# Performance work log

Hardware: AMD Instinct MI355X
Metric: run time of the kernel (lower is better)

The kernel has to match this reference:

```python
import jax, jax.numpy as jnp
import numpy as np

B, L, D, H, S = 2, 2048, 1024, 16, 4
Dh = D // H
EPS = 1e-5


def setup_inputs() -> dict:
    key = jax.random.key(0)
    ks = jax.random.split(key, 12)
    sc = 0.02
    w = lambda k, shape: (jax.random.normal(k, shape, jnp.float32) * sc)
    M = 2 * S  # number of MHA blocks / dense linears
    inp = {
        "response": jax.random.normal(ks[0], (B, L, D), jnp.float32),
        "mask": jnp.broadcast_to(jnp.tril(jnp.ones((L, L), bool)), (B, L, L)),
        "Wq": w(ks[1], (M, D, D)), "bq": w(ks[2], (M, D)),
        "Wk": w(ks[3], (M, D, D)), "bk": w(ks[4], (M, D)),
        "Wv": w(ks[5], (M, D, D)), "bv": w(ks[6], (M, D)),
        "Wo": w(ks[7], (M, D, D)), "bo": w(ks[8], (M, D)),
        "Wd": w(ks[9], (M, D, D)), "bd": w(ks[10], (M, D)),
    }
    return inp


def _ln(x):
    # fresh LayerNorm(d) with default weight=1, bias=0, eps=1e-5
    m = jnp.mean(x, axis=-1, keepdims=True)
    v = jnp.mean((x - m) ** 2, axis=-1, keepdims=True)
    return (x - m) * jax.lax.rsqrt(v + EPS)


def _linear(x, W, b):
    # torch Linear: x @ W.T + b
    return jnp.einsum('bld,od->blo', x, W) + b


def _mha(x, i, mask, Wq, bq, Wk, bk, Wv, bv, Wo, bo):
    # self-attention: q = k = v = x
    split = lambda y: y.reshape(B, L, H, Dh).transpose(0, 2, 1, 3)  # (B,H,L,Dh)
    q = split(_linear(x, Wq[i], bq[i]))
    k = split(_linear(x, Wk[i], bk[i]))
    v = split(_linear(x, Wv[i], bv[i]))
    scores = jnp.einsum('bhqd,bhkd->bhqk', q, k) / jnp.sqrt(jnp.float32(Dh))
    if mask is not None:
        scores = jnp.where(mask[:, None, :, :], scores, -jnp.inf)
    p = jnp.nan_to_num(jax.nn.softmax(scores, axis=-1))
    o = jnp.einsum('bhqk,bhkd->bhqd', p, v).transpose(0, 2, 1, 3).reshape(B, L, D)
    return _linear(o, Wo[i], bo[i])


def reference(response, mask, Wq, bq, Wk, bk, Wv, bv, Wo, bo, Wd, bd):
    x = response
    for i in range(S):
        # masked self-attention + residual + LN
        x = _ln(x + _mha(x, 2 * i, mask, Wq, bq, Wk, bk, Wv, bv, Wo, bo))
        # encoder-attention sublayer (encMem is None -> unmasked self-attention)
        x = _ln(x + _mha(x, 2 * i + 1, None, Wq, bq, Wk, bk, Wv, bv, Wo, bo))
        # dense: linear[2i](LeakyReLU(linear[2i+1](x)))
        h = jax.nn.leaky_relu(_linear(x, Wd[2 * i + 1], bd[2 * i + 1]), negative_slope=0.01)
        h = _linear(h, Wd[2 * i], bd[2 * i])
        x = _ln(x + h)
    return x
```

## Files before the change

kernel.cpp:

```cpp
#include <hip/hip_runtime.h>
#include <stdint.h>
#include <stddef.h>

typedef __attribute__((ext_vector_type(8))) _Float16 f16x8;
typedef __attribute__((ext_vector_type(4))) _Float16 f16x4;
typedef __attribute__((ext_vector_type(4))) float    f32x4;

#define NB 2
#define NL 2048
#define ND 1024
#define NH 16
#define NROWS (NB*NL)

__device__ __forceinline__ void async16(void* lds, const void* g) {
  __builtin_amdgcn_global_load_lds(
      (const __attribute__((address_space(1))) void*)g,
      (__attribute__((address_space(3))) void*)lds, 16, 0, 0);
}

struct CvtArgs { const float* in[6]; _Float16* out[6]; };

__global__ __launch_bounds__(256) void cvt_all(CvtArgs a, int n16, int rn16)
{
  const float* in  = a.in[blockIdx.z];
  _Float16*   out  = a.out[blockIdx.z];
  const int n = (blockIdx.z == 5) ? rn16 : n16;
  for (int i = blockIdx.x * blockDim.x + threadIdx.x; i < n;
       i += gridDim.x * blockDim.x) {
    const f32x4* src = (const f32x4*)in + 4 * (size_t)i;
    f32x4 v0 = __builtin_nontemporal_load(src);
    f32x4 v1 = __builtin_nontemporal_load(src + 1);
    f32x4 v2 = __builtin_nontemporal_load(src + 2);
    f32x4 v3 = __builtin_nontemporal_load(src + 3);
    f16x8 o0 = {(_Float16)v0[0], (_Float16)v0[1], (_Float16)v0[2], (_Float16)v0[3],
                (_Float16)v1[0], (_Float16)v1[1], (_Float16)v1[2], (_Float16)v1[3]};
    f16x8 o1 = {(_Float16)v2[0], (_Float16)v2[1], (_Float16)v2[2], (_Float16)v2[3],
                (_Float16)v3[0], (_Float16)v3[1], (_Float16)v3[2], (_Float16)v3[3]};
    __builtin_nontemporal_store(o0, (f16x8*)out + 2 * (size_t)i);
    __builtin_nontemporal_store(o1, (f16x8*)out + 2 * (size_t)i + 1);
  }
}

struct GArgs {
  const _Float16* A;
  const _Float16* B[3];
  const float*    bias[3];
  void*           out[3];
  int             mode[3];
  int             ksplit;
};

__global__ __launch_bounds__(256, 4) void gemm_bt(GArgs ga)
{
  __shared__ _Float16 As[128 * 64];
  __shared__ _Float16 Bs[128 * 64];
  const int tid = threadIdx.x;
  const int w = tid >> 6, l = tid & 63;
  const int ql = l & 15, g = l >> 4;
  const int z = blockIdx.z;
  const int widx = ga.ksplit ? 0 : (blockIdx.x >> 3);
  const _Float16* Bw  = ga.B[widx];
  const float*   bias = ga.bias[widx];
  void*          outp = ga.ksplit ? ga.out[z] : ga.out[widx];
  const int      mode = ga.mode[widx];
  const int kbeg = ga.ksplit ? z * (ND / 2) : 0;
  const int kend = ga.ksplit ? kbeg + ND / 2 : ND;
  const bool dobias = (!ga.ksplit) || (z == 0);
  const int brow = blockIdx.y * 128;
  const int bcol = (blockIdx.x & 7) * 128;
  const int wm = w >> 1, wn = w & 1;
  f32x4 acc[4][4] = {};

  const int srow = w * 32 + (l >> 3);
  const int scol = ((l & 7) ^ (l >> 3)) << 3;
  const _Float16* Ag = ga.A + (size_t)(brow + srow) * ND + scol;
  const _Float16* Bg = Bw   + (size_t)(bcol + srow) * ND + scol;

  for (int k0 = kbeg; k0 < kend; k0 += 64) {
    {
      _Float16* AsW = &As[w * 2048];
      _Float16* BsW = &Bs[w * 2048];
#pragma unroll
      for (int i = 0; i < 4; ++i) {
        async16(AsW + i * 512, Ag + (size_t)i * 8 * ND + k0);
        async16(BsW + i * 512, Bg + (size_t)i * 8 * ND + k0);
      }
    }
    asm volatile("s_waitcnt vmcnt(0)" ::: "memory");
    __builtin_amdgcn_s_barrier();
    __builtin_amdgcn_s_setprio(1);
#pragma unroll
    for (int ks = 0; ks < 64; ks += 32) {
      const int cx = (ks + g * 8) ^ ((ql & 7) << 3);
      f16x8 af[4], bf[4];
#pragma unroll
      for (int mi = 0; mi < 4; ++mi)
        af[mi] = *(const f16x8*)&As[(wm * 64 + mi * 16 + ql) * 64 + cx];
#pragma unroll
      for (int nj = 0; nj < 4; ++nj)
        bf[nj] = *(const f16x8*)&Bs[(wn * 64 + nj * 16 + ql) * 64 + cx];
#pragma unroll
      for (int mi = 0; mi < 4; ++mi)
#pragma unroll
        for (int nj = 0; nj < 4; ++nj)
          acc[mi][nj] = __builtin_amdgcn_mfma_f32_16x16x32_f16(
              af[mi], bf[nj], acc[mi][nj], 0, 0, 0);
    }
    __builtin_amdgcn_s_setprio(0);
    asm volatile("s_waitcnt lgkmcnt(0)" ::: "memory");
    __builtin_amdgcn_s_barrier();
  }

  const int colb = bcol + wn * 64;
  const int rowb = brow + wm * 64 + g * 4;
  if (mode == 3) {
    _Float16* vt = (_Float16*)outp;
    const int bb = rowb >> 11;
#pragma unroll
    for (int nj = 0; nj < 4; ++nj) {
      const int col = colb + nj * 16 + ql;
      const float bv = bias[col];
      const int hh = col >> 6, d = col & 63;
      _Float16* vrow = vt + ((size_t)((bb * NH + hh) * 64 + d)) * NL;
#pragma unroll
      for (int mi = 0; mi < 4; ++mi) {
        const int krow = (rowb + mi * 16) & (NL - 1);
        f16x4 o;
#pragma unroll
        for (int r = 0; r < 4; ++r) o[r] = (_Float16)(acc[mi][nj][r] + bv);
        *(f16x4*)(vrow + krow) = o;
      }
    }
  } else {
    _Float16* oh = (_Float16*)outp;
#pragma unroll
    for (int nj = 0; nj < 4; ++nj) {
      const int col = colb + nj * 16 + ql;
      const float bv = dobias ? bias[col] : 0.f;
#pragma unroll
      for (int mi = 0; mi < 4; ++mi) {
#pragma unroll
        for (int r = 0; r < 4; ++r) {
          float v = acc[mi][nj][r] + bv;
          if (mode == 2) v = v > 0.f ? v : 0.01f * v;
          oh[(size_t)(rowb + mi * 16 + r) * ND + col] = (_Float16)v;
        }
      }
    }
  }
}

template<bool CAUSAL>
__global__ __launch_bounds__(512, 4) void attn_fwd(
    const _Float16* __restrict__ Q, const _Float16* __restrict__ K,
    const _Float16* __restrict__ Vt, _Float16* __restrict__ O)
{
  __shared__ _Float16 kv[3][2][64 * 64];
  __shared__ unsigned int pls[8][8 * 34];
  const int tid = threadIdx.x;
  const int w = tid >> 6, l = tid & 63;
  const int ql = l & 15, g = l >> 4;
  const int bi = blockIdx.x;
  const int within = bi >> 3;
  const int p = (bi & 7) + 8 * (within >> 4);
  const int h = p & 15, b = p >> 4;
  const int qt_raw = within & 15;
  const int qt = (CAUSAL && b) ? (NL / 128 - 1 - qt_raw) : qt_raw;
  const int qrow = qt * 128 + w * 16 + ql;
  const int qmin = qt * 128 + w * 16;

  const _Float16* Qp = Q + (size_t)(b * NL + qrow) * ND + h * 64 + g * 8;
  const f16x8 bq0 = *(const f16x8*)Qp;
  const f16x8 bq1 = *(const f16x8*)(Qp + 32);

  const int srow = w * 8 + (l >> 3);
  const int scol = ((l & 7) ^ (l >> 3)) << 3;
  const _Float16* Kg = K  + ((size_t)(b * NL) + srow) * ND + h * 64 + scol;
  const _Float16* Vg = Vt + ((size_t)((b * NH + h) * 64 + srow)) * NL + scol;

  const int msk  = (ql & 7) << 3;
  const int offA = ql * 64 + ((     g * 8) ^ msk);
  const int offB = ql * 64 + ((32 + g * 8) ^ msk);

  unsigned int* pw = &pls[w][0];
  f32x4 ot[4] = {};
  f32x4 sum_acc = {};
  const f16x8 ones = {(_Float16)1.f, (_Float16)1.f, (_Float16)1.f, (_Float16)1.f,
                      (_Float16)1.f, (_Float16)1.f, (_Float16)1.f, (_Float16)1.f};
  const int ntiles = CAUSAL ? (qt * 2 + 2) : (NL / 64);
  const float SCL = 0.125f * 1.44269504089f;
  const float M2  = 4.0f * 1.44269504089f;

  async16(&kv[0][0][w * 512], Kg);
  async16(&kv[0][1][w * 512], Vg);

  int cbuf = 0, sbuf = 1;
  for (int kt = 0; kt < ntiles; ++kt) {
    const size_t nk0 = (size_t)((kt + 1 < ntiles) ? kt + 1 : kt) * 64;
    async16(&kv[sbuf][0][w * 512], Kg + nk0 * ND);
    async16(&kv[sbuf][1][w * 512], Vg + nk0);
    asm volatile("s_waitcnt vmcnt(2)" ::: "memory");
    __builtin_amdgcn_s_barrier();

    const _Float16* kb = &kv[cbuf][0][0];
    const _Float16* vb = &kv[cbuf][1][0];
    const int k0 = kt * 64;
    f32x4 st[4] = {};
    __builtin_amdgcn_s_setprio(1);
#pragma unroll
    for (int sub = 0; sub < 4; ++sub) {
      const f16x8 a0 = *(const f16x8*)&kb[sub * 1024 + offA];
      const f16x8 a1 = *(const f16x8*)&kb[sub * 1024 + offB];
      st[sub] = __builtin_amdgcn_mfma_f32_16x16x32_f16(a0, bq0, st[sub], 0, 0, 0);
      st[sub] = __builtin_amdgcn_mfma_f32_16x16x32_f16(a1, bq1, st[sub], 0, 0, 0);
    }
    __builtin_amdgcn_s_setprio(0);
    float pv[16];
    if (!CAUSAL || (k0 + 63 <= qmin)) {
#pragma unroll
      for (int sub = 0; sub < 4; ++sub)
#pragma unroll
        for (int r = 0; r < 4; ++r)
          pv[sub * 4 + r] = exp2f(__builtin_fmaf(st[sub][r], SCL, -M2));
    } else {
#pragma unroll
      for (int sub = 0; sub < 4; ++sub)
#pragma unroll
        for (int r = 0; r < 4; ++r) {
          float p2 = exp2f(__builtin_fmaf(st[sub][r], SCL, -M2));
          if ((k0 + sub * 16 + g * 4 + r) > qrow) p2 = 0.f;
          pv[sub * 4 + r] = p2;
        }
    }

#pragma unroll
    for (int sub = 0; sub < 2; ++sub) {
      uint2 uu;
      uu.x = __builtin_bit_cast(unsigned int,
                __builtin_amdgcn_cvt_pkrtz(pv[sub * 4 + 0], pv[sub * 4 + 1]));
      uu.y = __builtin_bit_cast(unsigned int,
                __builtin_amdgcn_cvt_pkrtz(pv[sub * 4 + 2], pv[sub * 4 + 3]));
      *(uint2*)&pw[(sub * 4 + g) * 34 + 2 * ql] = uu;
    }
    {
      uint2 lo = *(const uint2*)&pw[(2 * g    ) * 34 + 2 * ql];
      uint2 hi = *(const uint2*)&pw[(2 * g + 1) * 34 + 2 * ql];
      uint4 ui; ui.x = lo.x; ui.y = lo.y; ui.z = hi.x; ui.w = hi.y;
      const f16x8 pf = __builtin_bit_cast(f16x8, ui);
      __builtin_amdgcn_s_setprio(1);
#pragma unroll
      for (int dt = 0; dt < 4; ++dt) {
        const f16x8 vf = *(const f16x8*)&vb[dt * 1024 + offA];
        ot[dt] = __builtin_amdgcn_mfma_f32_16x16x32_f16(vf, pf, ot[dt], 0, 0, 0);
      }
      sum_acc = __builtin_amdgcn_mfma_f32_16x16x32_f16(ones, pf, sum_acc, 0, 0, 0);
      __builtin_amdgcn_s_setprio(0);
    }
#pragma unroll
    for (int sub = 2; sub < 4; ++sub) {
      uint2 uu;
      uu.x = __builtin_bit_cast(unsigned int,
                __builtin_amdgcn_cvt_pkrtz(pv[sub * 4 + 0], pv[sub * 4 + 1]));
      uu.y = __builtin_bit_cast(unsigned int,
                __builtin_amdgcn_cvt_pkrtz(pv[sub * 4 + 2], pv[sub * 4 + 3]));
      *(uint2*)&pw[((sub - 2) * 4 + g) * 34 + 2 * ql] = uu;
    }
    {
      uint2 lo = *(const uint2*)&pw[(2 * g    ) * 34 + 2 * ql];
      uint2 hi = *(const uint2*)&pw[(2 * g + 1) * 34 + 2 * ql];
      uint4 ui; ui.x = lo.x; ui.y = lo.y; ui.z = hi.x; ui.w = hi.y;
      const f16x8 pf = __builtin_bit_cast(f16x8, ui);
      __builtin_amdgcn_s_setprio(1);
#pragma unroll
      for (int dt = 0; dt < 4; ++dt) {
        const f16x8 vf = *(const f16x8*)&vb[dt * 1024 + offB];
        ot[dt] = __builtin_amdgcn_mfma_f32_16x16x32_f16(vf, pf, ot[dt], 0, 0, 0);
      }
      sum_acc = __builtin_amdgcn_mfma_f32_16x16x32_f16(ones, pf, sum_acc, 0, 0, 0);
      __builtin_amdgcn_s_setprio(0);
    }
    cbuf = sbuf;
    sbuf = sbuf + 1 == 3 ? 0 : sbuf + 1;
  }

  const float inv = 1.f / sum_acc[0];
#pragma unroll
  for (int dt = 0; dt < 4; ++dt) {
    f16x4 o;
#pragma unroll
    for (int r = 0; r < 4; ++r) o[r] = (_Float16)(ot[dt][r] * inv);
    *(f16x4*)(O + (size_t)(b * NL + qrow) * ND + h * 64 + dt * 16 + g * 4) = o;
  }
}

template<bool FINAL>
__global__ __launch_bounds__(256) void resid_ln(
    const _Float16* __restrict__ xh_in, const _Float16* __restrict__ d0,
    const _Float16* __restrict__ d1,
    _Float16* __restrict__ xh_out, float* __restrict__ xf)
{
  const int row = blockIdx.x, tid = threadIdx.x;
  const f16x4 xv = ((const f16x4*)(xh_in + (size_t)row * ND))[tid];
  const f16x4 v0 = ((const f16x4*)(d0 + (size_t)row * ND))[tid];
  const f16x4 v1 = ((const f16x4*)(d1 + (size_t)row * ND))[tid];
  const float a = (float)xv[0] + (float)v0[0] + (float)v1[0];
  const float b = (float)xv[1] + (float)v0[1] + (float)v1[1];
  const float c = (float)xv[2] + (float)v0[2] + (float)v1[2];
  const float d = (float)xv[3] + (float)v0[3] + (float)v1[3];
  float s = a + b + c + d;
  float ss = a * a + b * b + c * c + d * d;
#pragma unroll
  for (int m = 1; m < 64; m <<= 1) {
    s  += __shfl_xor(s, m);
    ss += __shfl_xor(ss, m);
  }
  __shared__ float red[8];
  if ((tid & 63) == 0) { red[tid >> 6] = s; red[4 + (tid >> 6)] = ss; }
  __syncthreads();
  const float S  = red[0] + red[1] + red[2] + red[3];
  const float SS = red[4] + red[5] + red[6] + red[7];
  const float mean = S * (1.0f / ND);
  const float var  = SS * (1.0f / ND) - mean * mean;
  const float rstd = rsqrtf(fmaxf(var, 0.f) + 1e-5f);
  const float ya = (a - mean) * rstd, yb = (b - mean) * rstd;
  const float yc = (c - mean) * rstd, yd = (d - mean) * rstd;
  if (FINAL) {
    float4 y; y.x = ya; y.y = yb; y.z = yc; y.w = yd;
    ((float4*)(xf + (size_t)row * ND))[tid] = y;
  } else {
    f16x4 yh = {(_Float16)ya, (_Float16)yb, (_Float16)yc, (_Float16)yd};
    ((f16x4*)(xh_out + (size_t)row * ND))[tid] = yh;
  }
}

extern "C" void kernel_launch(void* const* d_in, const int* in_sizes, int n_in,
                              void* d_out, int out_size, void* d_ws, size_t ws_size,
                              hipStream_t stream)
{
  (void)in_sizes; (void)n_in; (void)out_size; (void)ws_size;
  const float* response = (const float*)d_in[0];
  const float* Wq = (const float*)d_in[2];
  const float* bq = (const float*)d_in[3];
  const float* Wk = (const float*)d_in[4];
  const float* bk = (const float*)d_in[5];
  const float* Wv = (const float*)d_in[6];
  const float* bv = (const float*)d_in[7];
  const float* Wo = (const float*)d_in[8];
  const float* bo = (const float*)d_in[9];
  const float* Wd = (const float*)d_in[10];
  const float* bd = (const float*)d_in[11];
  float* xf = (float*)d_out;

  const size_t MB = 1024 * 1024;
  char* p = (char*)d_ws;
  _Float16* Wq_h = (_Float16*)(p + 0 * MB);
  _Float16* Wk_h = (_Float16*)(p + 16 * MB);
  _Float16* Wv_h = (_Float16*)(p + 32 * MB);
  _Float16* Wo_h = (_Float16*)(p + 48 * MB);
  _Float16* Wd_h = (_Float16*)(p + 64 * MB);
  _Float16* xh   = (_Float16*)(p + 80 * MB);
  _Float16* Qh   = (_Float16*)(p + 88 * MB);
  _Float16* Kh   = (_Float16*)(p + 96 * MB);
  _Float16* Vth  = (_Float16*)(p + 104 * MB);
  _Float16* Oh   = (_Float16*)(p + 112 * MB);
  _Float16* h1   = Qh;
  _Float16* t0   = (_Float16*)(p + 96 * MB);
  _Float16* t1   = (_Float16*)(p + 104 * MB);

  const int wn16 = 8 * 1024 * 1024 / 16;
  const int rn16 = NROWS * ND / 16;
  CvtArgs ca = { { Wq, Wk, Wv, Wo, Wd, response },
                 { Wq_h, Wk_h, Wv_h, Wo_h, Wd_h, xh } };
  cvt_all<<<dim3(1024, 1, 6), 256, 0, stream>>>(ca, wn16, rn16);

  const dim3 g3(24, NROWS / 128, 1);
  const dim3 gs(8, NROWS / 128, 2);
  const dim3 gf(8, NROWS / 128, 1);
  const dim3 agrid(NL / 128 * NH * NB);

  for (int i = 0; i < 4; ++i) {
    for (int sub = 0; sub < 2; ++sub) {
      const int m = 2 * i + sub;
      const size_t wo = (size_t)m * MB;
      const size_t bf = (size_t)m * 1024;
      GArgs qkv = { xh,
                    { Wq_h + wo, Wk_h + wo, Wv_h + wo },
                    { bq + bf, bk + bf, bv + bf },
                    { Qh, Kh, Vth }, { 0, 0, 3 }, 0 };
      gemm_bt<<<g3, 256, 0, stream>>>(qkv);
      if (sub == 0) attn_fwd<true ><<<agrid, 512, 0, stream>>>(Qh, Kh, Vth, Oh);
      else          attn_fwd<false><<<agrid, 512, 0, stream>>>(Qh, Kh, Vth, Oh);
      GArgs oprj = { Oh,
                     { Wo_h + wo, nullptr, nullptr },
                     { bo + bf, nullptr, nullptr },
                     { t0, t1, nullptr }, { 0, 0, 0 }, 1 };
      gemm_bt<<<gs, 256, 0, stream>>>(oprj);
      resid_ln<false><<<NROWS, 256, 0, stream>>>(xh, t0, t1, xh, nullptr);
    }
    const size_t w1 = (size_t)(2 * i + 1) * MB, b1 = (size_t)(2 * i + 1) * 1024;
    const size_t w0 = (size_t)(2 * i) * MB,     b0 = (size_t)(2 * i) * 1024;
    GArgs f1 = { xh,
                 { Wd_h + w1, nullptr, nullptr },
                 { bd + b1, nullptr, nullptr },
                 { h1, nullptr, nullptr }, { 2, 0, 0 }, 0 };
    gemm_bt<<<gf, 256, 0, stream>>>(f1);
    GArgs f2 = { h1,
                 { Wd_h + w0, nullptr, nullptr },
                 { bd + b0, nullptr, nullptr },
                 { t0, t1, nullptr }, { 0, 0, 0 }, 1 };
    gemm_bt<<<gs, 256, 0, stream>>>(f2);
    if (i == 3) resid_ln<true ><<<NROWS, 256, 0, stream>>>(xh, t0, t1, nullptr, xf);
    else        resid_ln<false><<<NROWS, 256, 0, stream>>>(xh, t0, t1, xh, nullptr);
  }
}
```

Baseline: 1.184 ms.

## Process KV tiles in pairs with double-buffered pair prefetch in attention

The attention loop now handles two 64-key tiles per iteration. The two tiles share one vmcnt(0) wait and one barrier, and the next pair is prefetched into the other half of a 4-slot LDS buffer. The aim is to halve the number of barriers and waits per key and so reduce synchronisation overhead. It also drops the fast path that skipped masking on fully-visible causal tiles, so the causal mask compare now runs on every tile. The extra LDS buffer raises shared memory use, which may reduce occupancy under launch_bounds(512,4).

```diff
diff --git a/kernel.cpp b/kernel.cpp
--- a/kernel.cpp
+++ b/kernel.cpp
@@ -155,7 +155,7 @@
     const _Float16* __restrict__ Q, const _Float16* __restrict__ K,
     const _Float16* __restrict__ Vt, _Float16* __restrict__ O)
 {
-  __shared__ _Float16 kv[3][2][64 * 64];
+  __shared__ _Float16 kv[4][2][64 * 64];
   __shared__ unsigned int pls[8][8 * 34];
   const int tid = threadIdx.x;
   const int w = tid >> 6, l = tid & 63;
@@ -167,7 +167,6 @@
   const int qt_raw = within & 15;
   const int qt = (CAUSAL && b) ? (NL / 128 - 1 - qt_raw) : qt_raw;
   const int qrow = qt * 128 + w * 16 + ql;
-  const int qmin = qt * 128 + w * 16;
 
   const _Float16* Qp = Q + (size_t)(b * NL + qrow) * ND + h * 64 + g * 8;
   const f16x8 bq0 = *(const f16x8*)Qp;
@@ -188,99 +187,102 @@
   const f16x8 ones = {(_Float16)1.f, (_Float16)1.f, (_Float16)1.f, (_Float16)1.f,
                       (_Float16)1.f, (_Float16)1.f, (_Float16)1.f, (_Float16)1.f};
   const int ntiles = CAUSAL ? (qt * 2 + 2) : (NL / 64);
+  const int npairs = ntiles >> 1;
   const float SCL = 0.125f * 1.44269504089f;
   const float M2  = 4.0f * 1.44269504089f;
 
   async16(&kv[0][0][w * 512], Kg);
   async16(&kv[0][1][w * 512], Vg);
-
-  int cbuf = 0, sbuf = 1;
-  for (int kt = 0; kt < ntiles; ++kt) {
-    const size_t nk0 = (size_t)((kt + 1 < ntiles) ? kt + 1 : kt) * 64;
-    async16(&kv[sbuf][0][w * 512], Kg + nk0 * ND);
-    async16(&kv[sbuf][1][w * 512], Vg + nk0);
-    asm volatile("s_waitcnt vmcnt(2)" ::: "memory");
+  async16(&kv[1][0][w * 512], Kg + (size_t)64 * ND);
+  async16(&kv[1][1][w * 512], Vg + 64);
+
+  int half = 0;
+  for (int pr = 0; pr < npairs; ++pr) {
+    asm volatile("s_waitcnt vmcnt(0)" ::: "memory");
     __builtin_amdgcn_s_barrier();
-
-    const _Float16* kb = &kv[cbuf][0][0];
-    const _Float16* vb = &kv[cbuf][1][0];
-    const int k0 = kt * 64;
-    f32x4 st[4] = {};
-    __builtin_amdgcn_s_setprio(1);
-#pragma unroll
-    for (int sub = 0; sub < 4; ++sub) {
-      const f16x8 a0 = *(const f16x8*)&kb[sub * 1024 + offA];
-      const f16x8 a1 = *(const f16x8*)&kb[sub * 1024 + offB];
-      st[sub] = __builtin_amdgcn_mfma_f32_16x16x32_f16(a0, bq0, st[sub], 0, 0, 0);
-      st[sub] = __builtin_amdgcn_mfma_f32_16x16x32_f16(a1, bq1, st[sub], 0, 0, 0);
-    }
-    __builtin_amdgcn_s_setprio(0);
-    float pv[16];
-    if (!CAUSAL || (k0 + 63 <= qmin)) {
-#pragma unroll
-      for (int sub = 0; sub < 4; ++sub)
-#pragma unroll
-        for (int r = 0; r < 4; ++r)
-          pv[sub * 4 + r] = exp2f(__builtin_fmaf(st[sub][r], SCL, -M2));
-    } else {
+    {
+      const int nh = half ^ 2;
+      const int np = (pr + 1 < npairs) ? pr + 1 : pr;
+      const size_t t0 = (size_t)(2 * np) * 64;
+      async16(&kv[nh    ][0][w * 512], Kg + t0 * ND);
+      async16(&kv[nh    ][1][w * 512], Vg + t0);
+      async16(&kv[nh + 1][0][w * 512], Kg + (t0 + 64) * ND);
+      async16(&kv[nh + 1][1][w * 512], Vg + t0 + 64);
+    }
+
+#pragma unroll
+    for (int t = 0; t < 2; ++t) {
+      const _Float16* kb = &kv[half + t][0][0];
+      const _Float16* vb = &kv[half + t][1][0];
+      const int k0 = (2 * pr + t) * 64;
+      f32x4 st[4] = {};
+      __builtin_amdgcn_s_setprio(1);
+#pragma unroll
+      for (int sub = 0; sub < 4; ++sub) {
+        const f16x8 a0 = *(const f16x8*)&kb[sub * 1024 + offA];
+        const f16x8 a1 = *(const f16x8*)&kb[sub * 1024 + offB];
+        st[sub] = __builtin_amdgcn_mfma_f32_16x16x32_f16(a0, bq0, st[sub], 0, 0, 0);
+        st[sub] = __builtin_amdgcn_mfma_f32_16x16x32_f16(a1, bq1, st[sub], 0, 0, 0);
+      }
+      __builtin_amdgcn_s_setprio(0);
+      float pv[16];
 #pragma unroll
       for (int sub = 0; sub < 4; ++sub)
 #pragma unroll
         for (int r = 0; r < 4; ++r) {
           float p2 = exp2f(__builtin_fmaf(st[sub][r], SCL, -M2));
-          if ((k0 + sub * 16 + g * 4 + r) > qrow) p2 = 0.f;
+          if (CAUSAL && (k0 + sub * 16 + g * 4 + r) > qrow) p2 = 0.f;
           pv[sub * 4 + r] = p2;
         }
-    }
-
-#pragma unroll
-    for (int sub = 0; sub < 2; ++sub) {
-      uint2 uu;
-      uu.x = __builtin_bit_cast(unsigned int,
-                __builtin_amdgcn_cvt_pkrtz(pv[sub * 4 + 0], pv[sub * 4 + 1]));
-      uu.y = __builtin_bit_cast(unsigned int,
-                __builtin_amdgcn_cvt_pkrtz(pv[sub * 4 + 2], pv[sub * 4 + 3]));
-      *(uint2*)&pw[(sub * 4 + g) * 34 + 2 * ql] = uu;
-    }
-    {
-      uint2 lo = *(const uint2*)&pw[(2 * g    ) * 34 + 2 * ql];
-      uint2 hi = *(const uint2*)&pw[(2 * g + 1) * 34 + 2 * ql];
-      uint4 ui; ui.x = lo.x; ui.y = lo.y; ui.z = hi.x; ui.w = hi.y;
-      const f16x8 pf = __builtin_bit_cast(f16x8, ui);
-      __builtin_amdgcn_s_setprio(1);
-#pragma unroll
-      for (int dt = 0; dt < 4; ++dt) {
-        const f16x8 vf = *(const f16x8*)&vb[dt * 1024 + offA];
-        ot[dt] = __builtin_amdgcn_mfma_f32_16x16x32_f16(vf, pf, ot[dt], 0, 0, 0);
-      }
-      sum_acc = __builtin_amdgcn_mfma_f32_16x16x32_f16(ones, pf, sum_acc, 0, 0, 0);
-      __builtin_amdgcn_s_setprio(0);
-    }
-#pragma unroll
-    for (int sub = 2; sub < 4; ++sub) {
-      uint2 uu;
-      uu.x = __builtin_bit_cast(unsigned int,
-                __builtin_amdgcn_cvt_pkrtz(pv[sub * 4 + 0], pv[sub * 4 + 1]));
-      uu.y = __builtin_bit_cast(unsigned int,
-                __builtin_amdgcn_cvt_pkrtz(pv[sub * 4 + 2], pv[sub * 4 + 3]));
-      *(uint2*)&pw[((sub - 2) * 4 + g) * 34 + 2 * ql] = uu;
-    }
-    {
-      uint2 lo = *(const uint2*)&pw[(2 * g    ) * 34 + 2 * ql];
-      uint2 hi = *(const uint2*)&pw[(2 * g + 1) * 34 + 2 * ql];
-      uint4 ui; ui.x = lo.x; ui.y = lo.y; ui.z = hi.x; ui.w = hi.y;
-      const f16x8 pf = __builtin_bit_cast(f16x8, ui);
-      __builtin_amdgcn_s_setprio(1);
-#pragma unroll
-      for (int dt = 0; dt < 4; ++dt) {
-        const f16x8 vf = *(const f16x8*)&vb[dt * 1024 + offB];
-        ot[dt] = __builtin_amdgcn_mfma_f32_16x16x32_f16(vf, pf, ot[dt], 0, 0, 0);
-      }
-      sum_acc = __builtin_amdgcn_mfma_f32_16x16x32_f16(ones, pf, sum_acc, 0, 0, 0);
-      __builtin_amdgcn_s_setprio(0);
-    }
-    cbuf = sbuf;
-    sbuf = sbuf + 1 == 3 ? 0 : sbuf + 1;
+
+#pragma unroll
+      for (int sub = 0; sub < 2; ++sub) {
+        uint2 uu;
+        uu.x = __builtin_bit_cast(unsigned int,
+                  __builtin_amdgcn_cvt_pkrtz(pv[sub * 4 + 0], pv[sub * 4 + 1]));
+        uu.y = __builtin_bit_cast(unsigned int,
+                  __builtin_amdgcn_cvt_pkrtz(pv[sub * 4 + 2], pv[sub * 4 + 3]));
+        *(uint2*)&pw[(sub * 4 + g) * 34 + 2 * ql] = uu;
+      }
+      {
+        uint2 lo = *(const uint2*)&pw[(2 * g    ) * 34 + 2 * ql];
+        uint2 hi = *(const uint2*)&pw[(2 * g + 1) * 34 + 2 * ql];
+        uint4 ui; ui.x = lo.x; ui.y = lo.y; ui.z = hi.x; ui.w = hi.y;
+        const f16x8 pf = __builtin_bit_cast(f16x8, ui);
+        __builtin_amdgcn_s_setprio(1);
+#pragma unroll
+        for (int dt = 0; dt < 4; ++dt) {
+          const f16x8 vf = *(const f16x8*)&vb[dt * 1024 + offA];
+          ot[dt] = __builtin_amdgcn_mfma_f32_16x16x32_f16(vf, pf, ot[dt], 0, 0, 0);
+        }
+        sum_acc = __builtin_amdgcn_mfma_f32_16x16x32_f16(ones, pf, sum_acc, 0, 0, 0);
+        __builtin_amdgcn_s_setprio(0);
+      }
+#pragma unroll
+      for (int sub = 2; sub < 4; ++sub) {
+        uint2 uu;
+        uu.x = __builtin_bit_cast(unsigned int,
+                  __builtin_amdgcn_cvt_pkrtz(pv[sub * 4 + 0], pv[sub * 4 + 1]));
+        uu.y = __builtin_bit_cast(unsigned int,
+                  __builtin_amdgcn_cvt_pkrtz(pv[sub * 4 + 2], pv[sub * 4 + 3]));
+        *(uint2*)&pw[((sub - 2) * 4 + g) * 34 + 2 * ql] = uu;
+      }
+      {
+        uint2 lo = *(const uint2*)&pw[(2 * g    ) * 34 + 2 * ql];
+        uint2 hi = *(const uint2*)&pw[(2 * g + 1) * 34 + 2 * ql];
+        uint4 ui; ui.x = lo.x; ui.y = lo.y; ui.z = hi.x; ui.w = hi.y;
+        const f16x8 pf = __builtin_bit_cast(f16x8, ui);
+        __builtin_amdgcn_s_setprio(1);
+#pragma unroll
+        for (int dt = 0; dt < 4; ++dt) {
+          const f16x8 vf = *(const f16x8*)&vb[dt * 1024 + offB];
+          ot[dt] = __builtin_amdgcn_mfma_f32_16x16x32_f16(vf, pf, ot[dt], 0, 0, 0);
+        }
+        sum_acc = __builtin_amdgcn_mfma_f32_16x16x32_f16(ones, pf, sum_acc, 0, 0, 0);
+        __builtin_amdgcn_s_setprio(0);
+      }
+    }
+    half ^= 2;
   }
 
   const float inv = 1.f / sum_acc[0];
```

Result: slower. 1.220 ms (+3.1%).
